# Performance work log

Hardware: AMD Instinct MI355X
Metric: run time of the kernel (lower is better)

The kernel has to match this reference:

```python
import jax, jax.numpy as jnp
import numpy as np
from jax import lax

K = 9  # 3x3 kernel points


def _gather(feat, iy, ix):
    """feat: [B,C,H,W]; iy,ix: [B,K,H,W] int32. Zero padding outside bounds.
    Returns [B,C,K,H,W]."""
    B, C, H, W = feat.shape
    valid = ((iy >= 0) & (iy < H) & (ix >= 0) & (ix < W))
    iyc = jnp.clip(iy, 0, H - 1)
    ixc = jnp.clip(ix, 0, W - 1)
    flat = (iyc * W + ixc).reshape(B, 1, -1)            # [B,1,K*H*W]
    g = jnp.take_along_axis(feat.reshape(B, C, H * W), flat, axis=2)
    g = g.reshape(B, C, K, H, W)
    return g * valid[:, None].astype(feat.dtype)


def _bilinear(feat, ys, xs):
    """feat: [B,C,H,W]; ys,xs: [B,K,H,W] float sampling coords -> [B,C,K,H,W]."""
    y0 = jnp.floor(ys)
    x0 = jnp.floor(xs)
    wy = (ys - y0)[:, None]
    wx = (xs - x0)[:, None]
    y0i = y0.astype(jnp.int32)
    x0i = x0.astype(jnp.int32)
    y1i = y0i + 1
    x1i = x0i + 1
    v00 = _gather(feat, y0i, x0i)
    v01 = _gather(feat, y0i, x1i)
    v10 = _gather(feat, y1i, x0i)
    v11 = _gather(feat, y1i, x1i)
    return (v00 * (1 - wy) * (1 - wx) + v01 * (1 - wy) * wx
            + v10 * wy * (1 - wx) + v11 * wy * wx)


def _deform_layer(x, w_off, b_off, w, b, dilation=1):
    """Modulated deformable 3x3 conv, stride 1, padding=dilation (same size)."""
    B, C, H, W = x.shape
    # offset/mask conv (regular 3x3 conv, same padding)
    om = lax.conv_general_dilated(
        x, w_off, window_strides=(1, 1),
        padding=[(dilation, dilation), (dilation, dilation)],
        rhs_dilation=(dilation, dilation),
        dimension_numbers=('NCHW', 'OIHW', 'NCHW')) + b_off[None, :, None, None]
    off = om[:, :2 * K].reshape(B, K, 2, H, W)   # (dy, dx) per kernel point
    mask = jax.nn.sigmoid(om[:, 2 * K:])         # [B,K,H,W]
    dy = off[:, :, 0]
    dx = off[:, :, 1]
    # base kernel grid offsets (-d, 0, +d)
    ky, kx = jnp.meshgrid(jnp.arange(3), jnp.arange(3), indexing='ij')
    base_y = ((ky.reshape(-1) - 1) * dilation).astype(x.dtype)   # [K]
    base_x = ((kx.reshape(-1) - 1) * dilation).astype(x.dtype)
    gy = jnp.arange(H, dtype=x.dtype)
    gx = jnp.arange(W, dtype=x.dtype)
    ys = gy[None, None, :, None] + base_y[None, :, None, None] + dy  # [B,K,H,W]
    xs = gx[None, None, None, :] + base_x[None, :, None, None] + dx
    sampled = _bilinear(x, ys, xs) * mask[:, None]   # [B,C,K,H,W]
    wk = w.reshape(w.shape[0], w.shape[1], K)        # [O,I,K]
    out = jnp.einsum('bikhw,oik->bohw', sampled, wk) + b[None, :, None, None]
    return out


def setup_inputs() -> dict:
    key = jax.random.key(0)
    ks = jax.random.split(key, 16)
    B, C, H, W = 4, 256, 64, 64
    O = 256
    inp = {'x': jax.random.normal(ks[0], (B, C, H, W), jnp.float32)}
    chans = [(C, C), (C, O), (O, O)]  # layer i==num_layers-2 maps in->out
    for i, (ci, co) in enumerate(chans):
        k = jax.random.split(ks[i + 1], 4)
        # offset conv: 27 = 3*K channels (18 offsets + 9 masks); small init
        inp[f'w_off{i}'] = jax.random.normal(k[0], (3 * K, ci, 3, 3), jnp.float32) * 0.01
        inp[f'b_off{i}'] = jnp.zeros((3 * K,), jnp.float32)
        # deform conv weight: kaiming normal, fan_in = ci*K
        std = np.sqrt(2.0 / (ci * K)).astype(np.float32)
        inp[f'w{i}'] = jax.random.normal(k[1], (co, ci, 3, 3), jnp.float32) * std
        inp[f'b{i}'] = jnp.zeros((co,), jnp.float32)
    return inp


def reference(x, w_off0, b_off0, w0, b0, w_off1, b_off1, w1, b1,
              w_off2, b_off2, w2, b2):
    params = [(w_off0, b_off0, w0, b0),
              (w_off1, b_off1, w1, b1),
              (w_off2, b_off2, w2, b2)]
    for (wo, bo, w, b) in params:
        x = jax.nn.relu(_deform_layer(x, wo, bo, w, b, dilation=1))
    return x
```

## Files before the change

### kernel.cpp

```cpp
#include <hip/hip_runtime.h>
#include <math.h>

#define Bn 4
#define Cn 256
#define Hn 64
#define Wn 64
#define On 256
#define HWn 4096
#define Pn 16384
#define Kc 2304

#define LGKM0 0xc07f

typedef _Float16 half8 __attribute__((ext_vector_type(8)));
typedef float floatx4 __attribute__((ext_vector_type(4)));

__global__ void k_init(const float* __restrict__ x, _Float16* __restrict__ act0,
                       const float* __restrict__ w0, const float* __restrict__ w1,
                       const float* __restrict__ w2, const float* __restrict__ wo0,
                       const float* __restrict__ wo1, const float* __restrict__ wo2,
                       _Float16* __restrict__ wtp, _Float16* __restrict__ wbop) {
  int bx = blockIdx.x;
  int tid = threadIdx.x;
  if (bx < 4096) {
    __shared__ float tile[32][33];
    int cx = bx & 127, cy = (bx >> 7) & 7, b = bx >> 10;
    int c0 = cx * 32, r0 = cy * 32;
    int tx = tid & 31, ty = tid >> 5;
    const float* ib = x + (size_t)b * Cn * HWn;
    _Float16* ob = act0 + (size_t)b * Cn * HWn;
#pragma unroll
    for (int i = 0; i < 32; i += 8)
      tile[ty + i][tx] = ib[(size_t)(r0 + ty + i) * HWn + (c0 + tx)];
    __syncthreads();
#pragma unroll
    for (int i = 0; i < 32; i += 8)
      ob[(size_t)(c0 + ty + i) * Cn + (r0 + tx)] = (_Float16)tile[tx][ty + i];
  } else if (bx < 4864) {
    int b2 = bx - 4096;
    int l = b2 >> 8;
    int n = b2 & 255;
    const float* w = (l == 0) ? w0 : (l == 1) ? w1 : w2;
    _Float16* dst = wtp + (size_t)l * 256 * Kc;
    int g = n >> 4, col = n & 15;
    int cq = tid >> 6;
    int kk = tid & 63;
    int kq = kk >> 5;
    int k32 = kk & 31;
    int quad = k32 >> 3;
    int e = k32 & 7;
    const float* src = w + (size_t)n * 2304 + (size_t)tid * 9;
#pragma unroll
    for (int t = 0; t < 9; ++t) {
      int c = t * 4 + cq;
      size_t d = ((size_t)((c * 16 + g) * 2 + kq)) * 512 + (quad * 16 + col) * 8 + e;
      dst[d] = (_Float16)src[t];
    }
  } else {
    int b3 = bx - 4864;
    int l = b3 >> 5;
    int n = b3 & 31;
    const float* w = (l == 0) ? wo0 : (l == 1) ? wo1 : wo2;
    _Float16* dst = wbop + (size_t)l * 36 * 2048;
    int g = n >> 4, col = n & 15;
    int cw = tid >> 6;
    int r = tid & 63;
    int kq = r >> 5;
    int r2 = r & 31;
    int quad = r2 >> 3;
    int e = r2 & 7;
#pragma unroll
    for (int t = 0; t < 9; ++t) {
      int c = cw * 9 + t;
      size_t d = ((size_t)((c * 2 + g) * 2 + kq)) * 512 + (quad * 16 + col) * 8 + e;
      dst[d] = (n < 27) ? (_Float16)w[((size_t)n * 256 + tid) * 9 + t] : (_Float16)0.f;
    }
  }
}

__global__ __launch_bounds__(512) void k_layer(
    const _Float16* __restrict__ xh,
    const _Float16* __restrict__ wbop, const float* __restrict__ boff,
    const _Float16* __restrict__ wtp, const float* __restrict__ bias,
    _Float16* __restrict__ outh, float* __restrict__ outf) {
  __shared__ __align__(16) _Float16 As[2][64][72];
  __shared__ __align__(16) _Float16 Bs[2][16384];
  __shared__ __align__(16) _Float16 win[3 * 66 * 64];
  __shared__ __align__(16) float omS[64 * 33];
  __shared__ __align__(16) float sampS[64][9][8];

  int bid = blockIdx.x;
  int lb = ((bid & 7) << 5) + (bid >> 3);
  int p0 = lb * 64;
  int tid = threadIdx.x;
  int lane = tid & 63;
  int wave = tid >> 6;
  int quad = lane >> 4;
  int col = lane & 15;

  int ar = tid >> 3;
  int aci = (tid & 7) * 8;

  int yB = (p0 & 4095) >> 6;
  int bB = p0 >> 12;

  half8 zero8;
#pragma unroll
  for (int e = 0; e < 8; ++e) zero8[e] = (_Float16)0.f;

  int mi = wave >> 1;
  int ng = wave & 1;

  floatx4 acc1 = (floatx4){0.f, 0.f, 0.f, 0.f};
  half8 boA[2], boB[2];
#pragma unroll
  for (int kq = 0; kq < 2; ++kq) {
    boA[kq] = *(const half8*)(wbop + (size_t)(ng * 2 + kq) * 512 + lane * 8);
    boB[kq] = *(const half8*)(wbop + 2048 + (size_t)(ng * 2 + kq) * 512 + lane * 8);
  }

#pragma unroll 1
  for (int cg = 0; cg < 4; ++cg) {
    for (int e = tid; e < 1584; e += 512) {
      int seg = e & 7;
      int rowpx = e >> 3;
      int r = rowpx / 66;
      int px = rowpx - r * 66;
      int yy = yB + r - 1;
      int xx = px - 1;
      half8 v = zero8;
      if (((unsigned)yy < 64u) & ((unsigned)xx < 64u))
        v = *(const half8*)(xh + ((size_t)((bB * Hn + yy) * Wn + xx)) * Cn +
                            cg * 64 + seg * 8);
      int ba = (rowpx * 128 + seg * 16) ^ ((px & 7) << 4);
      *(half8*)((char*)win + ba) = v;
    }
    __syncthreads();

#pragma unroll
    for (int t = 0; t < 9; ++t) {
      int cp = cg * 9 + t;
      int dty = t / 3;
      int dtx = t % 3;
#pragma unroll
      for (int kq = 0; kq < 2; ++kq) {
        int pxw = mi * 16 + col + dtx;
        int ba = ((dty * 66 + pxw) * 128 + kq * 64 + quad * 16) ^ ((pxw & 7) << 4);
        half8 af = *(const half8*)((const char*)win + ba);
        acc1 = __builtin_amdgcn_mfma_f32_16x16x32_f16(
            af, (cp & 1) ? boB[kq] : boA[kq], acc1, 0, 0, 0);
      }
      if (cp + 2 < 36) {
        const _Float16* wob = wbop + (size_t)(cp + 2) * 2048;
#pragma unroll
        for (int kq = 0; kq < 2; ++kq) {
          half8 v2 = *(const half8*)(wob + (size_t)(ng * 2 + kq) * 512 + lane * 8);
          if (cp & 1) boB[kq] = v2; else boA[kq] = v2;
        }
      }
    }
    __syncthreads();
  }

  {
    int n1 = ng * 16 + col;
    if (n1 < 27) {
      float bb = boff[n1];
#pragma unroll
      for (int r = 0; r < 4; ++r)
        omS[(mi * 16 + quad * 4 + r) * 33 + n1] = acc1[r] + bb;
    }
  }
  __syncthreads();

  for (int e = tid; e < 576; e += 512) {
    int lp = e / 9;
    int k = e - lp * 9;
    int pp = p0 + lp;
    int bi = pp >> 12;
    int pyx = pp & 4095;
    int py = pyx >> 6, px = pyx & 63;

    float dy = omS[lp * 33 + 2 * k];
    float dx = omS[lp * 33 + 2 * k + 1];
    float m = 1.f / (1.f + expf(-omS[lp * 33 + 18 + k]));

    float ys = (float)(py + k / 3 - 1) + dy;
    float xs = (float)(px + k % 3 - 1) + dx;
    float y0f = floorf(ys), x0f = floorf(xs);
    float wy = ys - y0f, wx = xs - x0f;
    int y0 = (int)y0f, x0 = (int)x0f;
    int y1 = y0 + 1, x1 = x0 + 1;

    bool vy0 = (y0 >= 0) & (y0 < Hn);
    bool vy1 = (y1 >= 0) & (y1 < Hn);
    bool vx0 = (x0 >= 0) & (x0 < Wn);
    bool vx1 = (x1 >= 0) & (x1 < Wn);
    int y0c = min(max(y0, 0), Hn - 1), y1c = min(max(y1, 0), Hn - 1);
    int x0c = min(max(x0, 0), Wn - 1), x1c = min(max(x1, 0), Wn - 1);

    int base = bi * HWn;
    float* s = &sampS[lp][k][0];
    ((int*)s)[0] = (base + y0c * Wn + x0c) * Cn;
    ((int*)s)[1] = (base + y0c * Wn + x1c) * Cn;
    ((int*)s)[2] = (base + y1c * Wn + x0c) * Cn;
    ((int*)s)[3] = (base + y1c * Wn + x1c) * Cn;
    s[4] = (vy0 && vx0) ? m * (1.f - wy) * (1.f - wx) : 0.f;
    s[5] = (vy0 && vx1) ? m * (1.f - wy) * wx : 0.f;
    s[6] = (vy1 && vx0) ? m * wy * (1.f - wx) : 0.f;
    s[7] = (vy1 && vx1) ? m * wy * wx : 0.f;
  }
  __syncthreads();

  int mw = wave >> 2;
  int nw = wave & 3;

  float bj[4];
#pragma unroll
  for (int j = 0; j < 4; ++j) bj[j] = bias[(nw * 4 + j) * 16 + col];

  floatx4 acc[2][4];
#pragma unroll
  for (int i = 0; i < 2; ++i)
#pragma unroll
    for (int j = 0; j < 4; ++j) acc[i][j] = (floatx4){0.f, 0.f, 0.f, 0.f};

  half8 g00, g01, g10, g11;
  half8 bst0[4], bst1[4];
  int4 ofsC, ofsN;
  float4 wvC, wvN;

  ofsC = *(const int4*)&sampS[ar][0][0];
  wvC = *(const float4*)&sampS[ar][0][4];
  ofsN = ofsC; wvN = wvC;
  g00 = *(const half8*)(xh + (size_t)ofsC.x + aci);
  g01 = *(const half8*)(xh + (size_t)ofsC.y + aci);
  g10 = *(const half8*)(xh + (size_t)ofsC.z + aci);
  g11 = *(const half8*)(xh + (size_t)ofsC.w + aci);
#pragma unroll
  for (int q = 0; q < 4; ++q)
    bst0[q] = *(const half8*)(wtp + (size_t)(q * 512 + tid) * 8);
#pragma unroll
  for (int q = 0; q < 4; ++q)
    bst1[q] = *(const half8*)(wtp + 16384 + (size_t)(q * 512 + tid) * 8);

#pragma unroll 1
  for (int t = 0; t < 9; ++t) {
    if (t < 8) {
      ofsN = *(const int4*)&sampS[ar][t + 1][0];
      wvN = *(const float4*)&sampS[ar][t + 1][4];
    }
#pragma unroll
    for (int cc = 0; cc < 4; ++cc) {
      {
        _Float16 h00 = (_Float16)wvC.x, h01 = (_Float16)wvC.y;
        _Float16 h10 = (_Float16)wvC.z, h11 = (_Float16)wvC.w;
        half8 r;
#pragma unroll
        for (int e = 0; e < 8; ++e)
          r[e] = g00[e] * h00 + g01[e] * h01 + g10[e] * h10 + g11[e] * h11;
        *(half8*)&As[cc & 1][ar][aci] = r;
      }
#pragma unroll
      for (int q = 0; q < 4; ++q)
        *(half8*)&Bs[cc & 1][(q * 512 + tid) * 8] = (cc & 1) ? bst1[q] : bst0[q];
      if (cc < 3) {
        int ci = (cc + 1) * 64 + aci;
        g00 = *(const half8*)(xh + (size_t)ofsC.x + ci);
        g01 = *(const half8*)(xh + (size_t)ofsC.y + ci);
        g10 = *(const half8*)(xh + (size_t)ofsC.z + ci);
        g11 = *(const half8*)(xh + (size_t)ofsC.w + ci);
      } else if (t < 8) {
        g00 = *(const half8*)(xh + (size_t)ofsN.x + aci);
        g01 = *(const half8*)(xh + (size_t)ofsN.y + aci);
        g10 = *(const half8*)(xh + (size_t)ofsN.z + aci);
        g11 = *(const half8*)(xh + (size_t)ofsN.w + aci);
      }
      if (cc < 2 || t < 8) {
        const _Float16* wsrc = wtp + ((size_t)(4 * t) + cc + 2) * 16384;
#pragma unroll
        for (int q = 0; q < 4; ++q) {
          half8 v = *(const half8*)(wsrc + (size_t)(q * 512 + tid) * 8);
          if (cc & 1) bst1[q] = v; else bst0[q] = v;
        }
      }

      __builtin_amdgcn_s_waitcnt(LGKM0);
      __builtin_amdgcn_s_barrier();

      half8 af[2][2];
#pragma unroll
      for (int kq = 0; kq < 2; ++kq)
#pragma unroll
        for (int i = 0; i < 2; ++i)
          af[kq][i] =
              *(const half8*)&As[cc & 1][mw * 32 + i * 16 + col][kq * 32 + quad * 8];

      half8 bf[2][4];
#pragma unroll
      for (int kq = 0; kq < 2; ++kq)
#pragma unroll
        for (int j = 0; j < 4; ++j)
          bf[kq][j] =
              *(const half8*)&Bs[cc & 1][((nw * 4 + j) * 2 + kq) * 512 + lane * 8];

#pragma unroll
      for (int kq = 0; kq < 2; ++kq)
#pragma unroll
        for (int i = 0; i < 2; ++i)
#pragma unroll
          for (int j = 0; j < 4; ++j)
            acc[i][j] = __builtin_amdgcn_mfma_f32_16x16x32_f16(
                af[kq][i], bf[kq][j], acc[i][j], 0, 0, 0);
    }
    ofsC = ofsN;
    wvC = wvN;
  }

#pragma unroll
  for (int i = 0; i < 2; ++i)
#pragma unroll
    for (int j = 0; j < 4; ++j) {
      int n = (nw * 4 + j) * 16 + col;
      if (outf) {
        int pb = p0 + mw * 32 + i * 16 + quad * 4;
        int bi = pb >> 12;
        int pyx = pb & 4095;
        float4 v;
        v.x = fmaxf(acc[i][j][0] + bj[j], 0.f);
        v.y = fmaxf(acc[i][j][1] + bj[j], 0.f);
        v.z = fmaxf(acc[i][j][2] + bj[j], 0.f);
        v.w = fmaxf(acc[i][j][3] + bj[j], 0.f);
        *(float4*)(outf + ((size_t)(bi * On + n)) * HWn + pyx) = v;
      } else {
#pragma unroll
        for (int r = 0; r < 4; ++r) {
          int pp = p0 + mw * 32 + i * 16 + quad * 4 + r;
          float v = fmaxf(acc[i][j][r] + bj[j], 0.f);
          outh[(size_t)pp * On + n] = (_Float16)v;
        }
      }
    }
}

extern "C" void kernel_launch(void* const* d_in, const int* in_sizes, int n_in,
                              void* d_out, int out_size, void* d_ws, size_t ws_size,
                              hipStream_t stream) {
  (void)in_sizes; (void)n_in; (void)out_size; (void)ws_size;
  const float* x = (const float*)d_in[0];

  _Float16* act0h = (_Float16*)d_ws;
  _Float16* act1h = act0h + (size_t)Pn * Cn;
  _Float16* wbop  = act1h + (size_t)Pn * Cn;
  _Float16* wtp   = wbop + (size_t)3 * 36 * 2048;

  k_init<<<4960, 256, 0, stream>>>(
      x, act0h,
      (const float*)d_in[3], (const float*)d_in[7], (const float*)d_in[11],
      (const float*)d_in[1], (const float*)d_in[5], (const float*)d_in[9],
      wtp, wbop);

  _Float16* cur = act0h;
  _Float16* nxt = act1h;
  for (int l = 0; l < 3; ++l) {
    const float* b_off = (const float*)d_in[2 + l * 4];
    const float* b     = (const float*)d_in[4 + l * 4];
    k_layer<<<Pn / 64, 512, 0, stream>>>(
        cur, wbop + (size_t)l * 36 * 2048, b_off,
        wtp + (size_t)l * 256 * Kc, b, nxt,
        (l == 2) ? (float*)d_out : nullptr);
    _Float16* tswap = cur; cur = nxt; nxt = tswap;
  }
}
```

Before: 230.8 us.

## Fuse three layer launches into one persistent kernel with grid barrier

Replaces the three per-layer k_layer launches with a single k_net kernel that loops over layers and separates them with a software grid-wide barrier (an atomic counter reset in k_init). The aim is to remove the launch gaps and tail drain between layers. It relies on all 256 blocks being co-resident (256 CUs), otherwise the barrier deadlocks. Spin-waiting and fence overhead may eat some of the saved gap time.

```diff
diff --git a/kernel.cpp b/kernel.cpp
--- a/kernel.cpp
+++ b/kernel.cpp
@@ -19,9 +19,11 @@
                        const float* __restrict__ w0, const float* __restrict__ w1,
                        const float* __restrict__ w2, const float* __restrict__ wo0,
                        const float* __restrict__ wo1, const float* __restrict__ wo2,
-                       _Float16* __restrict__ wtp, _Float16* __restrict__ wbop) {
+                       _Float16* __restrict__ wtp, _Float16* __restrict__ wbop,
+                       unsigned* __restrict__ bar) {
   int bx = blockIdx.x;
   int tid = threadIdx.x;
+  if (bx == 0 && tid == 0) atomicExch(bar, 0u);
   if (bx < 4096) {
     __shared__ float tile[32][33];
     int cx = bx & 127, cy = (bx >> 7) & 7, b = bx >> 10;
@@ -78,11 +80,13 @@
   }
 }
 
-__global__ __launch_bounds__(512) void k_layer(
-    const _Float16* __restrict__ xh,
-    const _Float16* __restrict__ wbop, const float* __restrict__ boff,
-    const _Float16* __restrict__ wtp, const float* __restrict__ bias,
-    _Float16* __restrict__ outh, float* __restrict__ outf) {
+__global__ __launch_bounds__(512) void k_net(
+    _Float16* __restrict__ act0, _Float16* __restrict__ act1,
+    const _Float16* __restrict__ wbop_all, const _Float16* __restrict__ wtp_all,
+    const float* __restrict__ boff0, const float* __restrict__ bias0,
+    const float* __restrict__ boff1, const float* __restrict__ bias1,
+    const float* __restrict__ boff2, const float* __restrict__ bias2,
+    float* __restrict__ dout, unsigned* __restrict__ bar) {
   __shared__ __align__(16) _Float16 As[2][64][72];
   __shared__ __align__(16) _Float16 Bs[2][16384];
   __shared__ __align__(16) _Float16 win[3 * 66 * 64];
@@ -108,239 +112,266 @@
 #pragma unroll
   for (int e = 0; e < 8; ++e) zero8[e] = (_Float16)0.f;
 
-  int mi = wave >> 1;
-  int ng = wave & 1;
-
-  floatx4 acc1 = (floatx4){0.f, 0.f, 0.f, 0.f};
-  half8 boA[2], boB[2];
-#pragma unroll
-  for (int kq = 0; kq < 2; ++kq) {
-    boA[kq] = *(const half8*)(wbop + (size_t)(ng * 2 + kq) * 512 + lane * 8);
-    boB[kq] = *(const half8*)(wbop + 2048 + (size_t)(ng * 2 + kq) * 512 + lane * 8);
+  const _Float16* cur = act0;
+  _Float16* nxt = act1;
+
+#pragma unroll 1
+  for (int l = 0; l < 3; ++l) {
+    const _Float16* wbop = wbop_all + (size_t)l * 36 * 2048;
+    const _Float16* wtp = wtp_all + (size_t)l * 256 * Kc;
+    const float* boff = (l == 0) ? boff0 : (l == 1) ? boff1 : boff2;
+    const float* bias = (l == 0) ? bias0 : (l == 1) ? bias1 : bias2;
+    float* outf = (l == 2) ? dout : nullptr;
+    const _Float16* xh = cur;
+    _Float16* outh = nxt;
+
+    int mi = wave >> 1;
+    int ng = wave & 1;
+
+    floatx4 acc1 = (floatx4){0.f, 0.f, 0.f, 0.f};
+    half8 boA[2], boB[2];
+#pragma unroll
+    for (int kq = 0; kq < 2; ++kq) {
+      boA[kq] = *(const half8*)(wbop + (size_t)(ng * 2 + kq) * 512 + lane * 8);
+      boB[kq] = *(const half8*)(wbop + 2048 + (size_t)(ng * 2 + kq) * 512 + lane * 8);
+    }
+
+#pragma unroll 1
+    for (int cg = 0; cg < 4; ++cg) {
+      for (int e = tid; e < 1584; e += 512) {
+        int seg = e & 7;
+        int rowpx = e >> 3;
+        int r = rowpx / 66;
+        int px = rowpx - r * 66;
+        int yy = yB + r - 1;
+        int xx = px - 1;
+        half8 v = zero8;
+        if (((unsigned)yy < 64u) & ((unsigned)xx < 64u))
+          v = *(const half8*)(xh + ((size_t)((bB * Hn + yy) * Wn + xx)) * Cn +
+                              cg * 64 + seg * 8);
+        int ba = (rowpx * 128 + seg * 16) ^ ((px & 7) << 4);
+        *(half8*)((char*)win + ba) = v;
+      }
+      __syncthreads();
+
+#pragma unroll
+      for (int t = 0; t < 9; ++t) {
+        int cp = cg * 9 + t;
+        int dty = t / 3;
+        int dtx = t % 3;
+#pragma unroll
+        for (int kq = 0; kq < 2; ++kq) {
+          int pxw = mi * 16 + col + dtx;
+          int ba = ((dty * 66 + pxw) * 128 + kq * 64 + quad * 16) ^ ((pxw & 7) << 4);
+          half8 af = *(const half8*)((const char*)win + ba);
+          acc1 = __builtin_amdgcn_mfma_f32_16x16x32_f16(
+              af, (cp & 1) ? boB[kq] : boA[kq], acc1, 0, 0, 0);
+        }
+        if (cp + 2 < 36) {
+          const _Float16* wob = wbop + (size_t)(cp + 2) * 2048;
+#pragma unroll
+          for (int kq = 0; kq < 2; ++kq) {
+            half8 v2 = *(const half8*)(wob + (size_t)(ng * 2 + kq) * 512 + lane * 8);
+            if (cp & 1) boB[kq] = v2; else boA[kq] = v2;
+          }
+        }
+      }
+      __syncthreads();
+    }
+
+    {
+      int n1 = ng * 16 + col;
+      if (n1 < 27) {
+        float bb = boff[n1];
+#pragma unroll
+        for (int r = 0; r < 4; ++r)
+          omS[(mi * 16 + quad * 4 + r) * 33 + n1] = acc1[r] + bb;
+      }
+    }
+    __syncthreads();
+
+    for (int e = tid; e < 576; e += 512) {
+      int lp = e / 9;
+      int k = e - lp * 9;
+      int pp = p0 + lp;
+      int bi = pp >> 12;
+      int pyx = pp & 4095;
+      int py = pyx >> 6, px = pyx & 63;
+
+      float dy = omS[lp * 33 + 2 * k];
+      float dx = omS[lp * 33 + 2 * k + 1];
+      float m = 1.f / (1.f + expf(-omS[lp * 33 + 18 + k]));
+
+      float ys = (float)(py + k / 3 - 1) + dy;
+      float xs = (float)(px + k % 3 - 1) + dx;
+      float y0f = floorf(ys), x0f = floorf(xs);
+      float wy = ys - y0f, wx = xs - x0f;
+      int y0 = (int)y0f, x0 = (int)x0f;
+      int y1 = y0 + 1, x1 = x0 + 1;
+
+      bool vy0 = (y0 >= 0) & (y0 < Hn);
+      bool vy1 = (y1 >= 0) & (y1 < Hn);
+      bool vx0 = (x0 >= 0) & (x0 < Wn);
+      bool vx1 = (x1 >= 0) & (x1 < Wn);
+      int y0c = min(max(y0, 0), Hn - 1), y1c = min(max(y1, 0), Hn - 1);
+      int x0c = min(max(x0, 0), Wn - 1), x1c = min(max(x1, 0), Wn - 1);
+
+      int base = bi * HWn;
+      float* s = &sampS[lp][k][0];
+      ((int*)s)[0] = (base + y0c * Wn + x0c) * Cn;
+      ((int*)s)[1] = (base + y0c * Wn + x1c) * Cn;
+      ((int*)s)[2] = (base + y1c * Wn + x0c) * Cn;
+      ((int*)s)[3] = (base + y1c * Wn + x1c) * Cn;
+      s[4] = (vy0 && vx0) ? m * (1.f - wy) * (1.f - wx) : 0.f;
+      s[5] = (vy0 && vx1) ? m * (1.f - wy) * wx : 0.f;
+      s[6] = (vy1 && vx0) ? m * wy * (1.f - wx) : 0.f;
+      s[7] = (vy1 && vx1) ? m * wy * wx : 0.f;
+    }
+    __syncthreads();
+
+    int mw = wave >> 2;
+    int nw = wave & 3;
+
+    float bj[4];
+#pragma unroll
+    for (int j = 0; j < 4; ++j) bj[j] = bias[(nw * 4 + j) * 16 + col];
+
+    floatx4 acc[2][4];
+#pragma unroll
+    for (int i = 0; i < 2; ++i)
+#pragma unroll
+      for (int j = 0; j < 4; ++j) acc[i][j] = (floatx4){0.f, 0.f, 0.f, 0.f};
+
+    half8 g00, g01, g10, g11;
+    half8 bst0[4], bst1[4];
+    int4 ofsC, ofsN;
+    float4 wvC, wvN;
+
+    ofsC = *(const int4*)&sampS[ar][0][0];
+    wvC = *(const float4*)&sampS[ar][0][4];
+    ofsN = ofsC; wvN = wvC;
+    g00 = *(const half8*)(xh + (size_t)ofsC.x + aci);
+    g01 = *(const half8*)(xh + (size_t)ofsC.y + aci);
+    g10 = *(const half8*)(xh + (size_t)ofsC.z + aci);
+    g11 = *(const half8*)(xh + (size_t)ofsC.w + aci);
+#pragma unroll
+    for (int q = 0; q < 4; ++q)
+      bst0[q] = *(const half8*)(wtp + (size_t)(q * 512 + tid) * 8);
+#pragma unroll
+    for (int q = 0; q < 4; ++q)
+      bst1[q] = *(const half8*)(wtp + 16384 + (size_t)(q * 512 + tid) * 8);
+
+#pragma unroll 1
+    for (int t = 0; t < 9; ++t) {
+      if (t < 8) {
+        ofsN = *(const int4*)&sampS[ar][t + 1][0];
+        wvN = *(const float4*)&sampS[ar][t + 1][4];
+      }
+#pragma unroll
+      for (int cc = 0; cc < 4; ++cc) {
+        {
+          _Float16 h00 = (_Float16)wvC.x, h01 = (_Float16)wvC.y;
+          _Float16 h10 = (_Float16)wvC.z, h11 = (_Float16)wvC.w;
+          half8 r;
+#pragma unroll
+          for (int e = 0; e < 8; ++e)
+            r[e] = g00[e] * h00 + g01[e] * h01 + g10[e] * h10 + g11[e] * h11;
+          *(half8*)&As[cc & 1][ar][aci] = r;
+        }
+#pragma unroll
+        for (int q = 0; q < 4; ++q)
+          *(half8*)&Bs[cc & 1][(q * 512 + tid) * 8] = (cc & 1) ? bst1[q] : bst0[q];
+        if (cc < 3) {
+          int ci = (cc + 1) * 64 + aci;
+          g00 = *(const half8*)(xh + (size_t)ofsC.x + ci);
+          g01 = *(const half8*)(xh + (size_t)ofsC.y + ci);
+          g10 = *(const half8*)(xh + (size_t)ofsC.z + ci);
+          g11 = *(const half8*)(xh + (size_t)ofsC.w + ci);
+        } else if (t < 8) {
+          g00 = *(const half8*)(xh + (size_t)ofsN.x + aci);
+          g01 = *(const half8*)(xh + (size_t)ofsN.y + aci);
+          g10 = *(const half8*)(xh + (size_t)ofsN.z + aci);
+          g11 = *(const half8*)(xh + (size_t)ofsN.w + aci);
+        }
+        if (cc < 2 || t < 8) {
+          const _Float16* wsrc = wtp + ((size_t)(4 * t) + cc + 2) * 16384;
+#pragma unroll
+          for (int q = 0; q < 4; ++q) {
+            half8 v = *(const half8*)(wsrc + (size_t)(q * 512 + tid) * 8);
+            if (cc & 1) bst1[q] = v; else bst0[q] = v;
+          }
+        }
+
+        __builtin_amdgcn_s_waitcnt(LGKM0);
+        __builtin_amdgcn_s_barrier();
+
+        half8 af[2][2];
+#pragma unroll
+        for (int kq = 0; kq < 2; ++kq)
+#pragma unroll
+          for (int i = 0; i < 2; ++i)
+            af[kq][i] =
+                *(const half8*)&As[cc & 1][mw * 32 + i * 16 + col][kq * 32 + quad * 8];
+
+        half8 bf[2][4];
+#pragma unroll
+        for (int kq = 0; kq < 2; ++kq)
+#pragma unroll
+          for (int j = 0; j < 4; ++j)
+            bf[kq][j] =
+                *(const half8*)&Bs[cc & 1][((nw * 4 + j) * 2 + kq) * 512 + lane * 8];
+
+#pragma unroll
+        for (int kq = 0; kq < 2; ++kq)
+#pragma unroll
+          for (int i = 0; i < 2; ++i)
+#pragma unroll
+            for (int j = 0; j < 4; ++j)
+              acc[i][j] = __builtin_amdgcn_mfma_f32_16x16x32_f16(
+                  af[kq][i], bf[kq][j], acc[i][j], 0, 0, 0);
+      }
+      ofsC = ofsN;
+      wvC = wvN;
+    }
+
+#pragma unroll
+    for (int i = 0; i < 2; ++i)
+#pragma unroll
+      for (int j = 0; j < 4; ++j) {
+        int n = (nw * 4 + j) * 16 + col;
+        if (outf) {
+          int pb = p0 + mw * 32 + i * 16 + quad * 4;
+          int bi = pb >> 12;
+          int pyx = pb & 4095;
+          float4 v;
+          v.x = fmaxf(acc[i][j][0] + bj[j], 0.f);
+          v.y = fmaxf(acc[i][j][1] + bj[j], 0.f);
+          v.z = fmaxf(acc[i][j][2] + bj[j], 0.f);
+          v.w = fmaxf(acc[i][j][3] + bj[j], 0.f);
+          *(float4*)(outf + ((size_t)(bi * On + n)) * HWn + pyx) = v;
+        } else {
+#pragma unroll
+          for (int r = 0; r < 4; ++r) {
+            int pp = p0 + mw * 32 + i * 16 + quad * 4 + r;
+            float v = fmaxf(acc[i][j][r] + bj[j], 0.f);
+            outh[(size_t)pp * On + n] = (_Float16)v;
+          }
+        }
+      }
+
+    if (l < 2) {
+      __threadfence();
+      __syncthreads();
+      if (tid == 0) {
+        atomicAdd(bar, 1u);
+        unsigned tgt = 256u * (unsigned)(l + 1);
+        while (atomicAdd(bar, 0u) < tgt) __builtin_amdgcn_s_sleep(2);
+      }
+      __syncthreads();
+      __threadfence();
+      _Float16* tsw = (_Float16*)cur; cur = nxt; nxt = tsw;
+    }
   }
-
-#pragma unroll 1
-  for (int cg = 0; cg < 4; ++cg) {
-    for (int e = tid; e < 1584; e += 512) {
-      int seg = e & 7;
-      int rowpx = e >> 3;
-      int r = rowpx / 66;
-      int px = rowpx - r * 66;
-      int yy = yB + r - 1;
-      int xx = px - 1;
-      half8 v = zero8;
-      if (((unsigned)yy < 64u) & ((unsigned)xx < 64u))
-        v = *(const half8*)(xh + ((size_t)((bB * Hn + yy) * Wn + xx)) * Cn +
-                            cg * 64 + seg * 8);
-      int ba = (rowpx * 128 + seg * 16) ^ ((px & 7) << 4);
-      *(half8*)((char*)win + ba) = v;
-    }
-    __syncthreads();
-
-#pragma unroll
-    for (int t = 0; t < 9; ++t) {
-      int cp = cg * 9 + t;
-      int dty = t / 3;
-      int dtx = t % 3;
-#pragma unroll
-      for (int kq = 0; kq < 2; ++kq) {
-        int pxw = mi * 16 + col + dtx;
-        int ba = ((dty * 66 + pxw) * 128 + kq * 64 + quad * 16) ^ ((pxw & 7) << 4);
-        half8 af = *(const half8*)((const char*)win + ba);
-        acc1 = __builtin_amdgcn_mfma_f32_16x16x32_f16(
-            af, (cp & 1) ? boB[kq] : boA[kq], acc1, 0, 0, 0);
-      }
-      if (cp + 2 < 36) {
-        const _Float16* wob = wbop + (size_t)(cp + 2) * 2048;
-#pragma unroll
-        for (int kq = 0; kq < 2; ++kq) {
-          half8 v2 = *(const half8*)(wob + (size_t)(ng * 2 + kq) * 512 + lane * 8);
-          if (cp & 1) boB[kq] = v2; else boA[kq] = v2;
-        }
-      }
-    }
-    __syncthreads();
-  }
-
-  {
-    int n1 = ng * 16 + col;
-    if (n1 < 27) {
-      float bb = boff[n1];
-#pragma unroll
-      for (int r = 0; r < 4; ++r)
-        omS[(mi * 16 + quad * 4 + r) * 33 + n1] = acc1[r] + bb;
-    }
-  }
-  __syncthreads();
-
-  for (int e = tid; e < 576; e += 512) {
-    int lp = e / 9;
-    int k = e - lp * 9;
-    int pp = p0 + lp;
-    int bi = pp >> 12;
-    int pyx = pp & 4095;
-    int py = pyx >> 6, px = pyx & 63;
-
-    float dy = omS[lp * 33 + 2 * k];
-    float dx = omS[lp * 33 + 2 * k + 1];
-    float m = 1.f / (1.f + expf(-omS[lp * 33 + 18 + k]));
-
-    float ys = (float)(py + k / 3 - 1) + dy;
-    float xs = (float)(px + k % 3 - 1) + dx;
-    float y0f = floorf(ys), x0f = floorf(xs);
-    float wy = ys - y0f, wx = xs - x0f;
-    int y0 = (int)y0f, x0 = (int)x0f;
-    int y1 = y0 + 1, x1 = x0 + 1;
-
-    bool vy0 = (y0 >= 0) & (y0 < Hn);
-    bool vy1 = (y1 >= 0) & (y1 < Hn);
-    bool vx0 = (x0 >= 0) & (x0 < Wn);
-    bool vx1 = (x1 >= 0) & (x1 < Wn);
-    int y0c = min(max(y0, 0), Hn - 1), y1c = min(max(y1, 0), Hn - 1);
-    int x0c = min(max(x0, 0), Wn - 1), x1c = min(max(x1, 0), Wn - 1);
-
-    int base = bi * HWn;
-    float* s = &sampS[lp][k][0];
-    ((int*)s)[0] = (base + y0c * Wn + x0c) * Cn;
-    ((int*)s)[1] = (base + y0c * Wn + x1c) * Cn;
-    ((int*)s)[2] = (base + y1c * Wn + x0c) * Cn;
-    ((int*)s)[3] = (base + y1c * Wn + x1c) * Cn;
-    s[4] = (vy0 && vx0) ? m * (1.f - wy) * (1.f - wx) : 0.f;
-    s[5] = (vy0 && vx1) ? m * (1.f - wy) * wx : 0.f;
-    s[6] = (vy1 && vx0) ? m * wy * (1.f - wx) : 0.f;
-    s[7] = (vy1 && vx1) ? m * wy * wx : 0.f;
-  }
-  __syncthreads();
-
-  int mw = wave >> 2;
-  int nw = wave & 3;
-
-  float bj[4];
-#pragma unroll
-  for (int j = 0; j < 4; ++j) bj[j] = bias[(nw * 4 + j) * 16 + col];
-
-  floatx4 acc[2][4];
-#pragma unroll
-  for (int i = 0; i < 2; ++i)
-#pragma unroll
-    for (int j = 0; j < 4; ++j) acc[i][j] = (floatx4){0.f, 0.f, 0.f, 0.f};
-
-  half8 g00, g01, g10, g11;
-  half8 bst0[4], bst1[4];
-  int4 ofsC, ofsN;
-  float4 wvC, wvN;
-
-  ofsC = *(const int4*)&sampS[ar][0][0];
-  wvC = *(const float4*)&sampS[ar][0][4];
-  ofsN = ofsC; wvN = wvC;
-  g00 = *(const half8*)(xh + (size_t)ofsC.x + aci);
-  g01 = *(const half8*)(xh + (size_t)ofsC.y + aci);
-  g10 = *(const half8*)(xh + (size_t)ofsC.z + aci);
-  g11 = *(const half8*)(xh + (size_t)ofsC.w + aci);
-#pragma unroll
-  for (int q = 0; q < 4; ++q)
-    bst0[q] = *(const half8*)(wtp + (size_t)(q * 512 + tid) * 8);
-#pragma unroll
-  for (int q = 0; q < 4; ++q)
-    bst1[q] = *(const half8*)(wtp + 16384 + (size_t)(q * 512 + tid) * 8);
-
-#pragma unroll 1
-  for (int t = 0; t < 9; ++t) {
-    if (t < 8) {
-      ofsN = *(const int4*)&sampS[ar][t + 1][0];
-      wvN = *(const float4*)&sampS[ar][t + 1][4];
-    }
-#pragma unroll
-    for (int cc = 0; cc < 4; ++cc) {
-      {
-        _Float16 h00 = (_Float16)wvC.x, h01 = (_Float16)wvC.y;
-        _Float16 h10 = (_Float16)wvC.z, h11 = (_Float16)wvC.w;
-        half8 r;
-#pragma unroll
-        for (int e = 0; e < 8; ++e)
-          r[e] = g00[e] * h00 + g01[e] * h01 + g10[e] * h10 + g11[e] * h11;
-        *(half8*)&As[cc & 1][ar][aci] = r;
-      }
-#pragma unroll
-      for (int q = 0; q < 4; ++q)
-        *(half8*)&Bs[cc & 1][(q * 512 + tid) * 8] = (cc & 1) ? bst1[q] : bst0[q];
-      if (cc < 3) {
-        int ci = (cc + 1) * 64 + aci;
-        g00 = *(const half8*)(xh + (size_t)ofsC.x + ci);
-        g01 = *(const half8*)(xh + (size_t)ofsC.y + ci);
-        g10 = *(const half8*)(xh + (size_t)ofsC.z + ci);
-        g11 = *(const half8*)(xh + (size_t)ofsC.w + ci);
-      } else if (t < 8) {
-        g00 = *(const half8*)(xh + (size_t)ofsN.x + aci);
-        g01 = *(const half8*)(xh + (size_t)ofsN.y + aci);
-        g10 = *(const half8*)(xh + (size_t)ofsN.z + aci);
-        g11 = *(const half8*)(xh + (size_t)ofsN.w + aci);
-      }
-      if (cc < 2 || t < 8) {
-        const _Float16* wsrc = wtp + ((size_t)(4 * t) + cc + 2) * 16384;
-#pragma unroll
-        for (int q = 0; q < 4; ++q) {
-          half8 v = *(const half8*)(wsrc + (size_t)(q * 512 + tid) * 8);
-          if (cc & 1) bst1[q] = v; else bst0[q] = v;
-        }
-      }
-
-      __builtin_amdgcn_s_waitcnt(LGKM0);
-      __builtin_amdgcn_s_barrier();
-
-      half8 af[2][2];
-#pragma unroll
-      for (int kq = 0; kq < 2; ++kq)
-#pragma unroll
-        for (int i = 0; i < 2; ++i)
-          af[kq][i] =
-              *(const half8*)&As[cc & 1][mw * 32 + i * 16 + col][kq * 32 + quad * 8];
-
-      half8 bf[2][4];
-#pragma unroll
-      for (int kq = 0; kq < 2; ++kq)
-#pragma unroll
-        for (int j = 0; j < 4; ++j)
-          bf[kq][j] =
-              *(const half8*)&Bs[cc & 1][((nw * 4 + j) * 2 + kq) * 512 + lane * 8];
-
-#pragma unroll
-      for (int kq = 0; kq < 2; ++kq)
-#pragma unroll
-        for (int i = 0; i < 2; ++i)
-#pragma unroll
-          for (int j = 0; j < 4; ++j)
-            acc[i][j] = __builtin_amdgcn_mfma_f32_16x16x32_f16(
-                af[kq][i], bf[kq][j], acc[i][j], 0, 0, 0);
-    }
-    ofsC = ofsN;
-    wvC = wvN;
-  }
-
-#pragma unroll
-  for (int i = 0; i < 2; ++i)
-#pragma unroll
-    for (int j = 0; j < 4; ++j) {
-      int n = (nw * 4 + j) * 16 + col;
-      if (outf) {
-        int pb = p0 + mw * 32 + i * 16 + quad * 4;
-        int bi = pb >> 12;
-        int pyx = pb & 4095;
-        float4 v;
-        v.x = fmaxf(acc[i][j][0] + bj[j], 0.f);
-        v.y = fmaxf(acc[i][j][1] + bj[j], 0.f);
-        v.z = fmaxf(acc[i][j][2] + bj[j], 0.f);
-        v.w = fmaxf(acc[i][j][3] + bj[j], 0.f);
-        *(float4*)(outf + ((size_t)(bi * On + n)) * HWn + pyx) = v;
-      } else {
-#pragma unroll
-        for (int r = 0; r < 4; ++r) {
-          int pp = p0 + mw * 32 + i * 16 + quad * 4 + r;
-          float v = fmaxf(acc[i][j][r] + bj[j], 0.f);
-          outh[(size_t)pp * On + n] = (_Float16)v;
-        }
-      }
-    }
 }
 
 extern "C" void kernel_launch(void* const* d_in, const int* in_sizes, int n_in,
@@ -353,22 +384,18 @@
   _Float16* act1h = act0h + (size_t)Pn * Cn;
   _Float16* wbop  = act1h + (size_t)Pn * Cn;
   _Float16* wtp   = wbop + (size_t)3 * 36 * 2048;
+  unsigned* bar   = (unsigned*)(wtp + (size_t)3 * 256 * Kc);
 
   k_init<<<4960, 256, 0, stream>>>(
       x, act0h,
       (const float*)d_in[3], (const float*)d_in[7], (const float*)d_in[11],
       (const float*)d_in[1], (const float*)d_in[5], (const float*)d_in[9],
-      wtp, wbop);
-
-  _Float16* cur = act0h;
-  _Float16* nxt = act1h;
-  for (int l = 0; l < 3; ++l) {
-    const float* b_off = (const float*)d_in[2 + l * 4];
-    const float* b     = (const float*)d_in[4 + l * 4];
-    k_layer<<<Pn / 64, 512, 0, stream>>>(
-        cur, wbop + (size_t)l * 36 * 2048, b_off,
-        wtp + (size_t)l * 256 * Kc, b, nxt,
-        (l == 2) ? (float*)d_out : nullptr);
-    _Float16* tswap = cur; cur = nxt; nxt = tswap;
-  }
+      wtp, wbop, bar);
+
+  k_net<<<256, 512, 0, stream>>>(
+      act0h, act1h, wbop, wtp,
+      (const float*)d_in[2], (const float*)d_in[4],
+      (const float*)d_in[6], (const float*)d_in[8],
+      (const float*)d_in[10], (const float*)d_in[12],
+      (float*)d_out, bar);
 }
```

Result: slower. 420.8 us (+82.3%).
